# Performance work log

Measured on AMD Instinct MI355X. Metric: run time of the kernel, lower is better.

The kernel has to match this reference:

```python
import jax, jax.numpy as jnp
import numpy as np

EPS = 1e-5  # torch BatchNorm2d default eps
B, C, H, W, G = 32, 256, 56, 56, 32


def setup_inputs() -> dict:
    key = jax.random.key(0)
    ks = jax.random.split(key, 12)
    x = jax.random.normal(ks[0], (B, C, H, W), dtype=jnp.float32)
    labels = jax.random.randint(ks[1], (B,), 0, 1000)
    # alpha_net: Conv2d(C, 1, 1) -> weight [1,C,1,1] flattened to [C], bias [1]
    alpha_w = jax.random.normal(ks[2], (C,), dtype=jnp.float32) * 0.05
    alpha_b = jnp.zeros((1,), dtype=jnp.float32)
    # global BatchNorm2d (eval mode: affine + running stats)
    g_w = 1.0 + 0.1 * jax.random.normal(ks[3], (C,), dtype=jnp.float32)
    g_b = 0.1 * jax.random.normal(ks[4], (C,), dtype=jnp.float32)
    g_rm = 0.1 * jax.random.normal(ks[5], (C,), dtype=jnp.float32)
    g_rv = 0.5 + jax.random.uniform(ks[6], (C,), dtype=jnp.float32)
    # per-group BatchNorm2d params, stacked [G, C]
    grp_w = 1.0 + 0.1 * jax.random.normal(ks[7], (G, C), dtype=jnp.float32)
    grp_b = 0.1 * jax.random.normal(ks[8], (G, C), dtype=jnp.float32)
    grp_rm = 0.1 * jax.random.normal(ks[9], (G, C), dtype=jnp.float32)
    grp_rv = 0.5 + jax.random.uniform(ks[10], (G, C), dtype=jnp.float32)
    return {"x": x, "labels": labels, "alpha_w": alpha_w, "alpha_b": alpha_b,
            "g_w": g_w, "g_b": g_b, "g_rm": g_rm, "g_rv": g_rv,
            "grp_w": grp_w, "grp_b": grp_b, "grp_rm": grp_rm, "grp_rv": grp_rv}


def reference(x, labels, alpha_w, alpha_b, g_w, g_b, g_rm, g_rv,
              grp_w, grp_b, grp_rm, grp_rv):
    # alpha gate: global avg pool -> 1x1 conv (C->1) -> sigmoid, per-sample scalar
    pooled = x.mean(axis=(2, 3))                       # [B, C]
    alpha = jax.nn.sigmoid(pooled @ alpha_w + alpha_b[0])  # [B]
    alpha = alpha[:, None, None, None]                 # [B,1,1,1]

    # global BN (eval): per-channel affine from running stats
    gs = g_w * jax.lax.rsqrt(g_rv + EPS)               # [C]
    gsh = g_b - g_rm * gs                              # [C]
    x_global = x * gs[None, :, None, None] + gsh[None, :, None, None]

    # eval path: mean over all G group BNs == single mean scale/shift per channel
    sg = grp_w * jax.lax.rsqrt(grp_rv + EPS)           # [G, C]
    ms = sg.mean(axis=0)                               # [C]
    msh = (grp_b - grp_rm * sg).mean(axis=0)           # [C]
    x_groups = x * ms[None, :, None, None] + msh[None, :, None, None]

    return (1.0 - alpha) * x_global + alpha * x_groups
```

## Files before the change

### kernel.cpp

```cpp
#include <hip/hip_runtime.h>
#include <math.h>

#define B_ 32
#define C_ 256
#define HW_ 3136
#define HW4_ 784
#define G_ 32
#define EPS_ 1e-5f

#define WS_POOL 0
#define WS_GS   (B_ * C_)
#define WS_GSH  (B_ * C_ + C_)
#define WS_MS   (B_ * C_ + 2 * C_)
#define WS_MSH  (B_ * C_ + 3 * C_)

__global__ __launch_bounds__(256) void pool_kernel(
    const float* __restrict__ x,
    const float* __restrict__ g_w, const float* __restrict__ g_b,
    const float* __restrict__ g_rm, const float* __restrict__ g_rv,
    const float* __restrict__ grp_w, const float* __restrict__ grp_b,
    const float* __restrict__ grp_rm, const float* __restrict__ grp_rv,
    float* __restrict__ ws) {
    const int bc = blockIdx.x;
    const int c  = bc & (C_ - 1);
    const int b  = bc >> 8;
    const int tid = threadIdx.x;

    const float4* __restrict__ p = (const float4*)(x + (size_t)bc * HW_);
    float s = 0.f;
    for (int i = tid; i < HW4_; i += 256) {
        float4 v = p[i];
        s += v.x + v.y + v.z + v.w;
    }
    #pragma unroll
    for (int off = 32; off; off >>= 1) s += __shfl_down(s, off);
    __shared__ float red[4];
    const int lane = tid & 63, wv = tid >> 6;
    if (lane == 0) red[wv] = s;
    __syncthreads();
    if (tid == 0) {
        ws[WS_POOL + bc] = (red[0] + red[1] + red[2] + red[3]) * (1.f / HW_);
    }

    if (b == 0 && tid < G_) {
        const int g = tid;
        float sg = grp_w[g * C_ + c] * rsqrtf(grp_rv[g * C_ + c] + EPS_);
        float sh = grp_b[g * C_ + c] - grp_rm[g * C_ + c] * sg;
        #pragma unroll
        for (int off = 16; off; off >>= 1) {
            sg += __shfl_down(sg, off);
            sh += __shfl_down(sh, off);
        }
        if (g == 0) {
            ws[WS_MS  + c] = sg * (1.f / G_);
            ws[WS_MSH + c] = sh * (1.f / G_);
            float gsv = g_w[c] * rsqrtf(g_rv[c] + EPS_);
            ws[WS_GS  + c] = gsv;
            ws[WS_GSH + c] = g_b[c] - g_rm[c] * gsv;
        }
    }
}

__global__ __launch_bounds__(256) void apply_kernel(
    const float* __restrict__ x,
    const float* __restrict__ ws,
    const float* __restrict__ alpha_w,
    const float* __restrict__ alpha_b,
    float* __restrict__ out) {
    const int bc = blockIdx.x;
    const int c  = bc & (C_ - 1);
    const int b  = bc >> 8;
    const int tid = threadIdx.x;

    float s = ws[WS_POOL + b * C_ + tid] * alpha_w[tid];
    #pragma unroll
    for (int off = 32; off; off >>= 1) s += __shfl_down(s, off);
    __shared__ float red[4];
    __shared__ float a_sh;
    const int lane = tid & 63, wv = tid >> 6;
    if (lane == 0) red[wv] = s;
    __syncthreads();
    if (tid == 0) {
        float z = red[0] + red[1] + red[2] + red[3] + alpha_b[0];
        a_sh = 1.f / (1.f + __expf(-z));
    }
    __syncthreads();
    const float a = a_sh;

    const float gs  = ws[WS_GS  + c], gsh = ws[WS_GSH + c];
    const float ms  = ws[WS_MS  + c], msh = ws[WS_MSH + c];
    const float sc = fmaf(a, ms - gs, gs);
    const float sh = fmaf(a, msh - gsh, gsh);

    const float4* __restrict__ px = (const float4*)(x + (size_t)bc * HW_);
    float4* __restrict__ po = (float4*)(out + (size_t)bc * HW_);
    for (int i = tid; i < HW4_; i += 256) {
        float4 v = px[i];
        float4 r;
        r.x = fmaf(v.x, sc, sh);
        r.y = fmaf(v.y, sc, sh);
        r.z = fmaf(v.z, sc, sh);
        r.w = fmaf(v.w, sc, sh);
        __builtin_nontemporal_store(r.x, &po[i].x);
        __builtin_nontemporal_store(r.y, &po[i].y);
        __builtin_nontemporal_store(r.z, &po[i].z);
        __builtin_nontemporal_store(r.w, &po[i].w);
    }
}

extern "C" void kernel_launch(void* const* d_in, const int* in_sizes, int n_in,
                              void* d_out, int out_size, void* d_ws, size_t ws_size,
                              hipStream_t stream) {
    const float* x       = (const float*)d_in[0];
    const float* alpha_w = (const float*)d_in[2];
    const float* alpha_b = (const float*)d_in[3];
    const float* g_w     = (const float*)d_in[4];
    const float* g_b     = (const float*)d_in[5];
    const float* g_rm    = (const float*)d_in[6];
    const float* g_rv    = (const float*)d_in[7];
    const float* grp_w   = (const float*)d_in[8];
    const float* grp_b   = (const float*)d_in[9];
    const float* grp_rm  = (const float*)d_in[10];
    const float* grp_rv  = (const float*)d_in[11];
    float* out = (float*)d_out;
    float* ws  = (float*)d_ws;

    pool_kernel<<<B_ * C_, 256, 0, stream>>>(x,
                                             g_w, g_b, g_rm, g_rv,
                                             grp_w, grp_b, grp_rm, grp_rv,
                                             ws);
    apply_kernel<<<B_ * C_, 256, 0, stream>>>(x, ws, alpha_w, alpha_b, out);
}
```

Measured before the change: 214.5 us.

## Fuse pool and apply into persistent kernel with per-image atomic counters

Replaces the separate pool and apply launches with one persistent kernel of 1024 blocks. Each block pools plane t, then applies plane t-1, and waits on a per-image atomic counter until all 256 channels of that image are pooled. The aim is to read each plane a second time while it is still cache-resident and to remove the launch gap between kernels. The cost is a memset launch, spin-waiting, and a deadlock risk if not all 1024 blocks are co-resident.

```diff
diff --git a/kernel.cpp b/kernel.cpp
--- a/kernel.cpp
+++ b/kernel.cpp
@@ -8,104 +8,111 @@
 #define G_ 32
 #define EPS_ 1e-5f
 
+#define GRID_ 1024
+#define PPB_ 8
+
 #define WS_POOL 0
-#define WS_GS   (B_ * C_)
-#define WS_GSH  (B_ * C_ + C_)
-#define WS_MS   (B_ * C_ + 2 * C_)
-#define WS_MSH  (B_ * C_ + 3 * C_)
+#define WS_CNT  (B_ * C_)
 
-__global__ __launch_bounds__(256) void pool_kernel(
+__global__ __launch_bounds__(256, 4) void fused_kernel(
     const float* __restrict__ x,
+    const float* __restrict__ alpha_w, const float* __restrict__ alpha_b,
     const float* __restrict__ g_w, const float* __restrict__ g_b,
     const float* __restrict__ g_rm, const float* __restrict__ g_rv,
     const float* __restrict__ grp_w, const float* __restrict__ grp_b,
     const float* __restrict__ grp_rm, const float* __restrict__ grp_rv,
-    float* __restrict__ ws) {
-    const int bc = blockIdx.x;
-    const int c  = bc & (C_ - 1);
-    const int b  = bc >> 8;
-    const int tid = threadIdx.x;
+    float* __restrict__ ws, float* __restrict__ out) {
+    const int tid  = threadIdx.x;
+    const int lane = tid & 63, wv = tid >> 6;
+    float* pooled = ws + WS_POOL;
+    unsigned int* cnt = (unsigned int*)(ws + WS_CNT);
 
-    const float4* __restrict__ p = (const float4*)(x + (size_t)bc * HW_);
-    float s = 0.f;
-    for (int i = tid; i < HW4_; i += 256) {
-        float4 v = p[i];
-        s += v.x + v.y + v.z + v.w;
+    __shared__ float red[4];
+    __shared__ float bcast[2];
+
+    auto pool_plane = [&](int p) {
+        const float4* __restrict__ px = (const float4*)(x + (size_t)p * HW_);
+        float s = 0.f;
+        for (int i = tid; i < HW4_; i += 256) {
+            float4 v = px[i];
+            s += v.x + v.y + v.z + v.w;
+        }
+        #pragma unroll
+        for (int off = 32; off; off >>= 1) s += __shfl_down(s, off);
+        if (lane == 0) red[wv] = s;
+        __syncthreads();
+        if (tid == 0) {
+            pooled[p] = (red[0] + red[1] + red[2] + red[3]) * (1.f / HW_);
+            __hip_atomic_fetch_add(&cnt[p >> 8], 1u,
+                                   __ATOMIC_RELEASE, __HIP_MEMORY_SCOPE_AGENT);
+        }
+        __syncthreads();
+    };
+
+    auto apply_plane = [&](int p) {
+        const int img = p >> 8, c = p & (C_ - 1);
+        if (tid == 0) {
+            while (__hip_atomic_load(&cnt[img], __ATOMIC_ACQUIRE,
+                                     __HIP_MEMORY_SCOPE_AGENT) < (unsigned)C_) {
+                __builtin_amdgcn_s_sleep(2);
+            }
+        }
+        __syncthreads();
+
+        float s = pooled[img * C_ + tid] * alpha_w[tid];
+        #pragma unroll
+        for (int off = 32; off; off >>= 1) s += __shfl_down(s, off);
+        if (lane == 0) red[wv] = s;
+        __syncthreads();
+
+        if (tid < G_) {
+            const int g = tid;
+            float sg = grp_w[g * C_ + c] * rsqrtf(grp_rv[g * C_ + c] + EPS_);
+            float sh = grp_b[g * C_ + c] - grp_rm[g * C_ + c] * sg;
+            #pragma unroll
+            for (int off = 16; off; off >>= 1) {
+                sg += __shfl_down(sg, off);
+                sh += __shfl_down(sh, off);
+            }
+            if (g == 0) {
+                float a   = 1.f / (1.f + __expf(-(red[0] + red[1] + red[2] + red[3]
+                                                  + alpha_b[0])));
+                float ms  = sg * (1.f / G_);
+                float msh = sh * (1.f / G_);
+                float gsv = g_w[c] * rsqrtf(g_rv[c] + EPS_);
+                float gsh = g_b[c] - g_rm[c] * gsv;
+                bcast[0] = fmaf(a, ms  - gsv, gsv);
+                bcast[1] = fmaf(a, msh - gsh, gsh);
+            }
+        }
+        __syncthreads();
+        const float sc = bcast[0], sh = bcast[1];
+
+        const float4* __restrict__ px = (const float4*)(x + (size_t)p * HW_);
+        float4* __restrict__ po = (float4*)(out + (size_t)p * HW_);
+        for (int i = tid; i < HW4_; i += 256) {
+            float4 v = px[i];
+            float4 r;
+            r.x = fmaf(v.x, sc, sh);
+            r.y = fmaf(v.y, sc, sh);
+            r.z = fmaf(v.z, sc, sh);
+            r.w = fmaf(v.w, sc, sh);
+            __builtin_nontemporal_store(r.x, &po[i].x);
+            __builtin_nontemporal_store(r.y, &po[i].y);
+            __builtin_nontemporal_store(r.z, &po[i].z);
+            __builtin_nontemporal_store(r.w, &po[i].w);
+        }
+        __syncthreads();
+    };
+
+    int prev = -1;
+    for (int t = 0; t < PPB_; ++t) {
+        const int p = t * GRID_ + blockIdx.x;
+        pool_plane(p);
+        if (prev >= 0) apply_plane(prev);
+        prev = p;
     }
-    #pragma unroll
-    for (int off = 32; off; off >>= 1) s += __shfl_down(s, off);
-    __shared__ float red[4];
-    const int lane = tid & 63, wv = tid >> 6;
-    if (lane == 0) red[wv] = s;
-    __syncthreads();
-    if (tid == 0) {
-        ws[WS_POOL + bc] = (red[0] + red[1] + red[2] + red[3]) * (1.f / HW_);
-    }
-
-    if (b == 0 && tid < G_) {
-        const int g = tid;
-        float sg = grp_w[g * C_ + c] * rsqrtf(grp_rv[g * C_ + c] + EPS_);
-        float sh = grp_b[g * C_ + c] - grp_rm[g * C_ + c] * sg;
-        #pragma unroll
-        for (int off = 16; off; off >>= 1) {
-            sg += __shfl_down(sg, off);
-            sh += __shfl_down(sh, off);
-        }
-        if (g == 0) {
-            ws[WS_MS  + c] = sg * (1.f / G_);
-            ws[WS_MSH + c] = sh * (1.f / G_);
-            float gsv = g_w[c] * rsqrtf(g_rv[c] + EPS_);
-            ws[WS_GS  + c] = gsv;
-            ws[WS_GSH + c] = g_b[c] - g_rm[c] * gsv;
-        }
-    }
-}
-
-__global__ __launch_bounds__(256) void apply_kernel(
-    const float* __restrict__ x,
-    const float* __restrict__ ws,
-    const float* __restrict__ alpha_w,
-    const float* __restrict__ alpha_b,
-    float* __restrict__ out) {
-    const int bc = blockIdx.x;
-    const int c  = bc & (C_ - 1);
-    const int b  = bc >> 8;
-    const int tid = threadIdx.x;
-
-    float s = ws[WS_POOL + b * C_ + tid] * alpha_w[tid];
-    #pragma unroll
-    for (int off = 32; off; off >>= 1) s += __shfl_down(s, off);
-    __shared__ float red[4];
-    __shared__ float a_sh;
-    const int lane = tid & 63, wv = tid >> 6;
-    if (lane == 0) red[wv] = s;
-    __syncthreads();
-    if (tid == 0) {
-        float z = red[0] + red[1] + red[2] + red[3] + alpha_b[0];
-        a_sh = 1.f / (1.f + __expf(-z));
-    }
-    __syncthreads();
-    const float a = a_sh;
-
-    const float gs  = ws[WS_GS  + c], gsh = ws[WS_GSH + c];
-    const float ms  = ws[WS_MS  + c], msh = ws[WS_MSH + c];
-    const float sc = fmaf(a, ms - gs, gs);
-    const float sh = fmaf(a, msh - gsh, gsh);
-
-    const float4* __restrict__ px = (const float4*)(x + (size_t)bc * HW_);
-    float4* __restrict__ po = (float4*)(out + (size_t)bc * HW_);
-    for (int i = tid; i < HW4_; i += 256) {
-        float4 v = px[i];
-        float4 r;
-        r.x = fmaf(v.x, sc, sh);
-        r.y = fmaf(v.y, sc, sh);
-        r.z = fmaf(v.z, sc, sh);
-        r.w = fmaf(v.w, sc, sh);
-        __builtin_nontemporal_store(r.x, &po[i].x);
-        __builtin_nontemporal_store(r.y, &po[i].y);
-        __builtin_nontemporal_store(r.z, &po[i].z);
-        __builtin_nontemporal_store(r.w, &po[i].w);
-    }
+    apply_plane(prev);
 }
 
 extern "C" void kernel_launch(void* const* d_in, const int* in_sizes, int n_in,
@@ -125,9 +132,11 @@
     float* out = (float*)d_out;
     float* ws  = (float*)d_ws;
 
-    pool_kernel<<<B_ * C_, 256, 0, stream>>>(x,
-                                             g_w, g_b, g_rm, g_rv,
-                                             grp_w, grp_b, grp_rm, grp_rv,
-                                             ws);
-    apply_kernel<<<B_ * C_, 256, 0, stream>>>(x, ws, alpha_w, alpha_b, out);
+    hipMemsetAsync((char*)d_ws + WS_CNT * sizeof(float), 0,
+                   B_ * sizeof(unsigned int), stream);
+
+    fused_kernel<<<GRID_, 256, 0, stream>>>(x, alpha_w, alpha_b,
+                                            g_w, g_b, g_rm, g_rv,
+                                            grp_w, grp_b, grp_rm, grp_rv,
+                                            ws, out);
 }
```

Result: slower. 718.3 us (+234.8%).
